# Performance work log

Hardware: AMD Instinct MI355X
Metric: run time of the kernel (lower is better)

The kernel has to match this reference:

```python
import jax, jax.numpy as jnp
import numpy as np

B, IN, OUT, G = 8192, 512, 512, 20


def setup_inputs() -> dict:
    key = jax.random.key(0)
    k1, k2, k3 = jax.random.split(key, 3)
    x = jax.random.normal(k1, (B, IN), dtype=jnp.float32)
    coeffs = jax.random.normal(k2, (OUT, IN, G + 1), dtype=jnp.float32) * 0.1
    base_w = jax.random.normal(k3, (OUT, IN), dtype=jnp.float32) * 0.1
    return {"x": x, "coeffs": coeffs, "base_w": base_w}


def reference(x, coeffs, base_w):
    g = coeffs.shape[-1] - 1  # grid_size
    xc = jnp.clip(x, -1.0, 1.0)
    base = jax.nn.silu(xc) @ base_w.T  # [B, out]
    x_grid = (xc + 1.0) * 0.5 * g  # [B, in], in [0, g]
    idx = jnp.clip(jnp.floor(x_grid).astype(jnp.int32), 0, g - 1)  # [B, in]
    t = x_grid - idx.astype(x.dtype)  # [B, in]
    b, n = x.shape
    bi = jnp.arange(b)[:, None]
    fi = jnp.arange(n)[None, :]
    # Sparse interpolation weights over grid bins: 2 nonzeros per (b, i).
    w = jnp.zeros((b, n, g + 1), dtype=x.dtype)
    w = w.at[bi, fi, idx].add(1.0 - t)
    w = w.at[bi, fi, idx + 1].add(t)  # idx+1 <= g since idx <= g-1
    # y[b,o] = sum_i sum_g w[b,i,g] * coeffs[o,i,g]
    y = jnp.einsum('big,oig->bo', w, coeffs)
    return base + y
```

## Files before the change

### kernel.cpp

```cpp
#include <hip/hip_runtime.h>
#include <stdint.h>


typedef short v8s __attribute__((ext_vector_type(8)));
typedef float v4f __attribute__((ext_vector_type(4)));

#define B_DIM 8192
#define IN_DIM 512
#define OUT_DIM 512
#define G_DIM 20
#define FPT 4
#define KT_TOTAL (IN_DIM / FPT)
#define KSPLIT 3
#define BM 128
#define BN 128
#define CHUNKS 12
#define PLANE 2048
#define TILE_BYTES (CHUNKS * PLANE)

#define P_BYTES ((size_t)IN_DIM * B_DIM * 8)
#define WT_BYTES ((size_t)(OUT_DIM / BN) * KT_TOTAL * TILE_BYTES)
#define PART_ELEMS ((size_t)B_DIM * OUT_DIM)
#define WS_NEED (P_BYTES + WT_BYTES + (size_t)KSPLIT * PART_ELEMS * 2)

#define PACK_BLKS ((B_DIM / 64) * (IN_DIM / 64))
#define WPACK_BLKS ((OUT_DIM * IN_DIM) / 256)

static __device__ __forceinline__ unsigned f2bf(float f) {
  unsigned u = __builtin_bit_cast(unsigned, f);
  return (u + 0x7fffu + ((u >> 16) & 1u)) >> 16;
}

static __device__ __forceinline__ float bflo(unsigned u) {
  return __builtin_bit_cast(float, u << 16);
}
static __device__ __forceinline__ float bfhi(unsigned u) {
  return __builtin_bit_cast(float, u & 0xffff0000u);
}

static __device__ __forceinline__ void load16(const void* g, void* l) {
  __builtin_amdgcn_global_load_lds(
      (const __attribute__((address_space(1))) unsigned*)g,
      (__attribute__((address_space(3))) unsigned*)l, 16, 0, 0);
}

__global__ void zero_out_kernel(uint4* __restrict__ out) {
  out[(size_t)blockIdx.x * 256 + threadIdx.x] = uint4{0u, 0u, 0u, 0u};
}

__global__ void pack_fused_kernel(const float* __restrict__ x, uint2* __restrict__ P,
                                  const float* __restrict__ coeffs,
                                  const float* __restrict__ base_w,
                                  char* __restrict__ Wt) {
  __shared__ uint2 tile[64 * 65];
  const int t = threadIdx.x;
  if (blockIdx.x < PACK_BLKS) {
    const int b0 = (blockIdx.x & (B_DIM / 64 - 1)) * 64;
    const int i0 = (blockIdx.x / (B_DIM / 64)) * 64;
    const int tr = t >> 6;
    const int tc = t & 63;
#pragma unroll
    for (int it = 0; it < 16; ++it) {
      int br = it * 4 + tr;
      float xv = x[(size_t)(b0 + br) * IN_DIM + i0 + tc];
      float xc = fminf(fmaxf(xv, -1.0f), 1.0f);
      float xg = (xc + 1.0f) * 10.0f;
      int idx = (int)floorf(xg);
      idx = idx < 0 ? 0 : (idx > G_DIM - 1 ? G_DIM - 1 : idx);
      float tt = xg - (float)idx;
      float sl = xc / (1.0f + __expf(-xc));
      uint2 pv;
      pv.x = f2bf(1.0f - tt) | (f2bf(tt) << 16);
      pv.y = (unsigned)idx | (f2bf(sl) << 16);
      tile[tc * 65 + br] = pv;
    }
    __syncthreads();
#pragma unroll
    for (int it = 0; it < 16; ++it) {
      int ir = it * 4 + tr;
      P[(size_t)(i0 + ir) * B_DIM + b0 + tc] = tile[ir * 65 + tc];
    }
  } else {
    const unsigned u = (blockIdx.x - PACK_BLKS) * 256 + t;
    const int s = u >> 9;
    const int w = u & 511;
    const int row = w >> 2;
    const int f = w & 3;
    const int n_blk = s / KT_TOTAL;
    const int kt = s - n_blk * KT_TOTAL;
    const int o = n_blk * 128 + row;
    const int i = kt * 4 + f;
    const size_t g = (size_t)o * IN_DIM + i;
    const float* c = coeffs + g * 21;
    float cf[21];
#pragma unroll
    for (int j = 0; j < 21; ++j) cf[j] = c[j];
    float bw = base_w[g];
    unsigned d[12];
#pragma unroll
    for (int j = 0; j < 10; ++j) d[j] = f2bf(cf[2 * j]) | (f2bf(cf[2 * j + 1]) << 16);
    d[10] = f2bf(cf[20]) | (f2bf(bw) << 16);
    d[11] = 0u;
    char* slab = Wt + (size_t)s * TILE_BYTES;
#pragma unroll
    for (int p = 0; p < 3; ++p)
      *(uint4*)(slab + (3 * f + p) * PLANE + row * 16) =
          uint4{d[4 * p], d[4 * p + 1], d[4 * p + 2], d[4 * p + 3]};
  }
}

__global__ void reduce_kernel(const uint4* __restrict__ p, v4f* __restrict__ out) {
  size_t i = (size_t)blockIdx.x * 256 + threadIdx.x;
  const size_t q = PART_ELEMS / 8;
  uint4 a = p[i], b = p[i + q], c = p[i + 2 * q];
  v4f lo, hi;
  lo[0] = bflo(a.x) + bflo(b.x) + bflo(c.x);
  hi[0] = bfhi(a.x) + bfhi(b.x) + bfhi(c.x);
  lo[1] = bflo(a.y) + bflo(b.y) + bflo(c.y);
  hi[1] = bfhi(a.y) + bfhi(b.y) + bfhi(c.y);
  lo[2] = bflo(a.z) + bflo(b.z) + bflo(c.z);
  hi[2] = bfhi(a.z) + bfhi(b.z) + bfhi(c.z);
  lo[3] = bflo(a.w) + bflo(b.w) + bflo(c.w);
  hi[3] = bfhi(a.w) + bfhi(b.w) + bfhi(c.w);
  v4f o0 = {lo[0], hi[0], lo[1], hi[1]};
  v4f o1 = {lo[2], hi[2], lo[3], hi[3]};
  out[2 * i] = o0;
  out[2 * i + 1] = o1;
}

static __device__ __forceinline__ void stage_strip(char* abase, uint2 pv) {
  const uint4 zz = {0u, 0u, 0u, 0u};
#pragma unroll
  for (int p = 0; p < 3; ++p) *(uint4*)(abase + p * PLANE) = zz;
  const int idx = (int)(pv.y & 0xffffu);
  const int s1 = idx + 1;
  *(unsigned short*)(abase + ((idx >> 3) << 11) + ((idx & 7) << 1)) =
      (unsigned short)pv.x;
  *(unsigned short*)(abase + ((s1 >> 3) << 11) + ((s1 & 7) << 1)) =
      (unsigned short)(pv.x >> 16);
  *(unsigned short*)(abase + 2 * PLANE + 10) = (unsigned short)(pv.y >> 16);
}

template <bool ATOMIC>
__global__ __launch_bounds__(256, 3) void kan_gemm(const uint2* __restrict__ P,
                                                   const char* __restrict__ Wt,
                                                   unsigned short* __restrict__ part,
                                                   float* __restrict__ outA) {
  __shared__ uint4 lds4[(2 * TILE_BYTES) / 16];
  char* Ab = (char*)lds4;
  char* Bb = (char*)lds4 + TILE_BYTES;
  const int t = threadIdx.x;
  const int lane = t & 63;
  const int wv = t >> 6;
  const int wm = wv >> 1, wn = wv & 1;
  const int b0 = blockIdx.x * BM;
  const int n_blk = blockIdx.y;
  const int z = blockIdx.z;
  const int kt0 = (z * KT_TOTAL) / KSPLIT;
  const int ktend = ((z + 1) * KT_TOTAL) / KSPLIT;

  v4f acc[4][4];
  const v4f z4 = {0.f, 0.f, 0.f, 0.f};
#pragma unroll
  for (int ii = 0; ii < 4; ++ii)
#pragma unroll
    for (int jj = 0; jj < 4; ++jj) acc[ii][jj] = z4;

  char* abase0 = Ab + 3 * wv * PLANE + lane * 16;
  char* abase1 = Ab + 3 * wv * PLANE + (lane + 64) * 16;
  uint2 pv0 = P[(size_t)(kt0 * 4 + wv) * B_DIM + b0 + lane];
  uint2 pv1 = P[(size_t)(kt0 * 4 + wv) * B_DIM + b0 + lane + 64];

  const int r16 = lane & 15;
  const int q16 = lane >> 4;

  for (int kt = kt0; kt < ktend; ++kt) {
    __syncthreads();

    const char* wsrc = Wt + (size_t)(n_blk * KT_TOTAL + kt) * TILE_BYTES;
#pragma unroll
    for (int q = 0; q < 6; ++q)
      load16(wsrc + (q * 256 + t) * 16, Bb + (q * 256 + t) * 16);

    const int ktn = (kt + 1 < ktend) ? kt + 1 : kt;
    uint2 pn0 = P[(size_t)(ktn * 4 + wv) * B_DIM + b0 + lane];
    uint2 pn1 = P[(size_t)(ktn * 4 + wv) * B_DIM + b0 + lane + 64];

    stage_strip(abase0, pv0);
    stage_strip(abase1, pv1);
    pv0 = pn0;
    pv1 = pn1;

    __syncthreads();

#pragma unroll
    for (int s = 0; s < 3; ++s) {
      const int chunk = s * 4 + q16;
      v8s af[4], bfr[4];
#pragma unroll
      for (int rm = 0; rm < 4; ++rm) {
        int row = wm * 64 + rm * 16 + r16;
        af[rm] = *(const v8s*)(Ab + chunk * PLANE + row * 16);
      }
#pragma unroll
      for (int cn = 0; cn < 4; ++cn) {
        int row = wn * 64 + cn * 16 + r16;
        bfr[cn] = *(const v8s*)(Bb + chunk * PLANE + row * 16);
      }
#pragma unroll
      for (int rm = 0; rm < 4; ++rm)
#pragma unroll
        for (int cn = 0; cn < 4; ++cn)
          acc[rm][cn] = __builtin_amdgcn_mfma_f32_16x16x32_bf16(af[rm], bfr[cn], acc[rm][cn], 0, 0, 0);
    }
  }

  const int q4 = (lane >> 4) * 4;
  if (ATOMIC) {
#pragma unroll
    for (int rm = 0; rm < 4; ++rm)
#pragma unroll
      for (int cn = 0; cn < 4; ++cn)
#pragma unroll
        for (int r = 0; r < 4; ++r) {
          int row = b0 + wm * 64 + rm * 16 + q4 + r;
          int col = n_blk * BN + wn * 64 + cn * 16 + r16;
          atomicAdd(outA + (size_t)row * OUT_DIM + col, acc[rm][cn][r]);
        }
  } else {
    unsigned short* mypart = part + (size_t)z * PART_ELEMS;
#pragma unroll
    for (int rm = 0; rm < 4; ++rm)
#pragma unroll
      for (int cn = 0; cn < 4; ++cn)
#pragma unroll
        for (int r = 0; r < 4; ++r) {
          int row = b0 + wm * 64 + rm * 16 + q4 + r;
          int col = n_blk * BN + wn * 64 + cn * 16 + r16;
          mypart[(size_t)row * OUT_DIM + col] = (unsigned short)f2bf(acc[rm][cn][r]);
        }
  }
}

extern "C" void kernel_launch(void* const* d_in, const int* in_sizes, int n_in,
                              void* d_out, int out_size, void* d_ws, size_t ws_size,
                              hipStream_t stream) {
  const float* x = (const float*)d_in[0];
  const float* coeffs = (const float*)d_in[1];
  const float* base_w = (const float*)d_in[2];
  float* out = (float*)d_out;

  uint2* P = (uint2*)d_ws;
  char* Wt = (char*)d_ws + P_BYTES;
  unsigned short* part = (unsigned short*)((char*)d_ws + P_BYTES + WT_BYTES);

  pack_fused_kernel<<<PACK_BLKS + WPACK_BLKS, 256, 0, stream>>>(x, P, coeffs, base_w, Wt);

  if (ws_size >= WS_NEED) {
    kan_gemm<false><<<dim3(B_DIM / BM, OUT_DIM / BN, KSPLIT), 256, 0, stream>>>(P, Wt, part, out);
    reduce_kernel<<<(int)(PART_ELEMS / 8 / 256), 256, 0, stream>>>((const uint4*)part, (v4f*)out);
  } else {
    zero_out_kernel<<<(int)((PART_ELEMS * 4) / 4096), 256, 0, stream>>>((uint4*)out);
    kan_gemm<true><<<dim3(B_DIM / BM, OUT_DIM / BN, KSPLIT), 256, 0, stream>>>(P, Wt, part, out);
  }
}
```

Measured before the change: 194.1 us.

## Load B weight fragments directly from global into registers, bypassing LDS

The B operand (packed weight tiles) now goes straight from global memory into registers at each wave's fragment positions, instead of being staged in LDS with global_load_lds and then read back. This halves LDS use per block, which may allow more resident blocks, and removes the LDS round trip for B. In exchange, every wave loads its own B fragments, so global and L2 traffic for weights doubles (the two wm waves share columns). Register pressure also rises by 48 extra VGPRs holding bv, and the loads are issued inside the loop with little latency hiding.

```diff
diff --git a/kernel.cpp b/kernel.cpp
--- a/kernel.cpp
+++ b/kernel.cpp
@@ -36,12 +36,6 @@
 }
 static __device__ __forceinline__ float bfhi(unsigned u) {
   return __builtin_bit_cast(float, u & 0xffff0000u);
-}
-
-static __device__ __forceinline__ void load16(const void* g, void* l) {
-  __builtin_amdgcn_global_load_lds(
-      (const __attribute__((address_space(1))) unsigned*)g,
-      (__attribute__((address_space(3))) unsigned*)l, 16, 0, 0);
 }
 
 __global__ void zero_out_kernel(uint4* __restrict__ out) {
@@ -146,9 +140,8 @@
                                                    const char* __restrict__ Wt,
                                                    unsigned short* __restrict__ part,
                                                    float* __restrict__ outA) {
-  __shared__ uint4 lds4[(2 * TILE_BYTES) / 16];
+  __shared__ uint4 lds4[TILE_BYTES / 16];
   char* Ab = (char*)lds4;
-  char* Bb = (char*)lds4 + TILE_BYTES;
   const int t = threadIdx.x;
   const int lane = t & 63;
   const int wv = t >> 6;
@@ -174,13 +167,24 @@
   const int r16 = lane & 15;
   const int q16 = lane >> 4;
 
+  const uint4* wbase = (const uint4*)(Wt + (size_t)n_blk * KT_TOTAL * TILE_BYTES);
+  int bidx[3][4];
+#pragma unroll
+  for (int s = 0; s < 3; ++s)
+#pragma unroll
+    for (int cn = 0; cn < 4; ++cn)
+      bidx[s][cn] = (s * 4 + q16) * 128 + wn * 64 + cn * 16 + r16;
+
   for (int kt = kt0; kt < ktend; ++kt) {
     __syncthreads();
 
-    const char* wsrc = Wt + (size_t)(n_blk * KT_TOTAL + kt) * TILE_BYTES;
-#pragma unroll
-    for (int q = 0; q < 6; ++q)
-      load16(wsrc + (q * 256 + t) * 16, Bb + (q * 256 + t) * 16);
+    const uint4* wsrc = wbase + (size_t)kt * (TILE_BYTES / 16);
+    uint4 bv[3][4];
+#pragma unroll
+    for (int s = 0; s < 3; ++s)
+#pragma unroll
+      for (int cn = 0; cn < 4; ++cn)
+        bv[s][cn] = wsrc[bidx[s][cn]];
 
     const int ktn = (kt + 1 < ktend) ? kt + 1 : kt;
     uint2 pn0 = P[(size_t)(ktn * 4 + wv) * B_DIM + b0 + lane];
@@ -196,22 +200,18 @@
 #pragma unroll
     for (int s = 0; s < 3; ++s) {
       const int chunk = s * 4 + q16;
-      v8s af[4], bfr[4];
+      v8s af[4];
 #pragma unroll
       for (int rm = 0; rm < 4; ++rm) {
         int row = wm * 64 + rm * 16 + r16;
         af[rm] = *(const v8s*)(Ab + chunk * PLANE + row * 16);
       }
 #pragma unroll
-      for (int cn = 0; cn < 4; ++cn) {
-        int row = wn * 64 + cn * 16 + r16;
-        bfr[cn] = *(const v8s*)(Bb + chunk * PLANE + row * 16);
-      }
-#pragma unroll
       for (int rm = 0; rm < 4; ++rm)
 #pragma unroll
         for (int cn = 0; cn < 4; ++cn)
-          acc[rm][cn] = __builtin_amdgcn_mfma_f32_16x16x32_bf16(af[rm], bfr[cn], acc[rm][cn], 0, 0, 0);
+          acc[rm][cn] = __builtin_amdgcn_mfma_f32_16x16x32_bf16(
+              af[rm], __builtin_bit_cast(v8s, bv[s][cn]), acc[rm][cn], 0, 0, 0);
     }
   }
 
```

Result: faster. 180.5 us (-7.0%).
